# Performance work log

Measured on AMD Instinct MI355X. Metric: run time of the kernel, lower is better.

The kernel has to match this reference:

```python
import jax, jax.numpy as jnp
import numpy as np

S, B, D, H, DH = 512, 32, 256, 8, 32  # seq, batch, in_dim, heads, dim_head
LN_EPS = 1e-5


def setup_inputs() -> dict:
    key = jax.random.key(0)
    k1, k2, k3 = jax.random.split(key, 3)
    x = jax.random.normal(k1, (S, B, D), jnp.float32)
    slow_W = jax.random.normal(k2, (H * (5 * DH + 2), D), jnp.float32) * 0.02
    out_W = jax.random.normal(k3, (D, H * DH), jnp.float32) * 0.02
    ln_g = jnp.ones((D,), jnp.float32)
    ln_b = jnp.zeros((D,), jnp.float32)
    return {"x": x, "slow_W": slow_W, "out_W": out_W, "ln_g": ln_g, "ln_b": ln_b}


def elu_p1(x):
    return jax.nn.elu(x) + 1.0


def sum_norm(x):
    return x / jnp.sum(x, axis=-1, keepdims=True)


def layer_norm(x, g, b):
    mu = jnp.mean(x, axis=-1, keepdims=True)
    var = jnp.mean(jnp.square(x - mu), axis=-1, keepdims=True)
    return (x - mu) * jax.lax.rsqrt(var + LN_EPS) * g + b


def _fast_rnn_forward(x, slow_W, out_W, ln_g, ln_b):
    slen, bsz, _ = x.shape
    o = layer_norm(x, ln_g, ln_b)
    qkv = jnp.einsum('sbd,ed->sbe', o, slow_W)  # [S,B,H*(5*DH+2)]
    qkv = qkv.reshape(slen, bsz, H, 5 * DH + 2)
    q, k, v, rk, rv, beta, rbeta = jnp.split(
        qkv, [DH, 2 * DH, 3 * DH, 4 * DH, 5 * DH, 5 * DH + 1], axis=-1)
    beta = jax.nn.sigmoid(beta)      # [S,B,H,1]
    rbeta = jax.nn.sigmoid(rbeta)    # [S,B,H,1]
    q = sum_norm(elu_p1(q))
    k = sum_norm(elu_p1(k))
    rk = jax.nn.softmax(rk, axis=-1)

    # ---- feed-forward fast weights with delta rule (fast_weight_delta) ----
    def ff_step(W, inp):
        qt, kt, vt, bt = inp                      # [B,H,DH], bt [B,H,1]
        v_old = jnp.einsum('bhij,bhj->bhi', W, kt)
        W = W + ((bt * (vt - v_old))[..., :, None] * kt[..., None, :])
        z = jnp.einsum('bhij,bhj->bhi', W, qt)
        return W, z

    W0 = jnp.zeros((bsz, H, DH, DH), x.dtype)
    _, z = jax.lax.scan(ff_step, W0, (q, k, v, beta))  # z: [S,B,H,DH]

    # ---- recurrent fast weights (fast_rnn_v2): query = softmax(prev state) ----
    def rec_step(carry, inp):
        R, h = carry
        zt, kt, vt, bt = inp
        q_rec = jax.nn.softmax(h, axis=-1)         # query from previous state
        v_old = jnp.einsum('bhij,bhj->bhi', R, kt)
        R = R + ((bt * (vt - v_old))[..., :, None] * kt[..., None, :])
        h = zt + jnp.einsum('bhij,bhj->bhi', R, q_rec)
        return (R, h), h

    R0 = jnp.zeros((bsz, H, DH, DH), x.dtype)
    h0 = jnp.zeros((bsz, H, DH), x.dtype)
    _, hs = jax.lax.scan(rec_step, (R0, h0), (z, rk, rv, rbeta))  # [S,B,H,DH]

    out = hs.reshape(slen, bsz, H * DH)
    out = jnp.einsum('sbe,de->sbd', out, out_W)
    return x + out  # dropout is identity in eval


def reference(x, slow_W, out_W, ln_g, ln_b):
    return _fast_rnn_forward(x, slow_W, out_W, ln_g, ln_b)
```

## Files before the change

kernel.cpp:

```cpp
#include <hip/hip_runtime.h>
#include <hip/hip_bf16.h>
#include <math.h>

#define S_   512
#define B_   32
#define D_   256
#define H_   8
#define DH_  32
#define E_   (H_*(5*DH_+2))
#define SB_  (S_*B_)
#define LN_EPSF 1e-5f

#define ROWP_ 164
#define CH2_  32
#define NC2_  (S_/CH2_)
#define NPAD_ 1344

typedef short  bf16x8 __attribute__((ext_vector_type(8)));
typedef float  f32x4  __attribute__((ext_vector_type(4)));

__device__ __forceinline__ float wave_sum64(float v){
  #pragma unroll
  for (int m = 32; m >= 1; m >>= 1) v += __shfl_xor(v, m, 64);
  return v;
}
__device__ __forceinline__ float gsum32(float v){
  #pragma unroll
  for (int m = 16; m >= 1; m >>= 1) v += __shfl_xor(v, m, 32);
  return v;
}
__device__ __forceinline__ float gmax32(float v){
  #pragma unroll
  for (int m = 16; m >= 1; m >>= 1) v = fmaxf(v, __shfl_xor(v, m, 32));
  return v;
}

#if __has_builtin(__builtin_amdgcn_permlane32_swap)
typedef int v2i_ __attribute__((ext_vector_type(2)));
__device__ __forceinline__ float xhalf_sum(float x){
  v2i_ r = __builtin_amdgcn_permlane32_swap(__float_as_int(x), __float_as_int(x), false, false);
  return __int_as_float(r.x) + __int_as_float(r.y);
}
#else
__device__ __forceinline__ float xhalf_sum(float x){
  return x + __shfl_xor(x, 32, 64);
}
#endif

__device__ __forceinline__ void gl16(const float* g, float* l){
  __builtin_amdgcn_global_load_lds(
      (const __attribute__((address_space(1))) unsigned int*)g,
      (__attribute__((address_space(3))) unsigned int*)l, 16, 0, 0);
}
__device__ __forceinline__ void stage_plane32(const float* gb, int fieldOff,
                                              float* plane, int lane){
  const int tt = lane >> 3, dd = (lane & 7) << 2;
  #pragma unroll
  for (int i = 0; i < 4; i++)
    gl16(gb + (size_t)(8*i + tt)*ROWP_ + fieldOff + dd, plane + i*256);
}
__device__ __forceinline__ void stage_beta32(const float* gb, float* bpl, int lane){
  if (lane < CH2_) gl16(gb + (size_t)lane*ROWP_ + 5*DH_, bpl);
}

__global__ __launch_bounds__(256) void ln_kernel(const float* __restrict__ x,
                                                 const float* __restrict__ g,
                                                 const float* __restrict__ b,
                                                 __hip_bfloat16* __restrict__ o){
  __shared__ float sbuf[4];
  const int row = blockIdx.x, tid = threadIdx.x;
  const float v = x[(size_t)row*D_ + tid];
  float s = wave_sum64(v);
  if ((tid & 63) == 0) sbuf[tid >> 6] = s;
  __syncthreads();
  const float mu = (sbuf[0]+sbuf[1]+sbuf[2]+sbuf[3]) * (1.f/D_);
  __syncthreads();
  const float d = v - mu;
  float s2 = wave_sum64(d*d);
  if ((tid & 63) == 0) sbuf[tid >> 6] = s2;
  __syncthreads();
  const float var = (sbuf[0]+sbuf[1]+sbuf[2]+sbuf[3]) * (1.f/D_);
  const float rstd = rsqrtf(var + LN_EPSF);
  o[(size_t)row*D_ + tid] = __float2bfloat16(d*rstd*g[tid] + b[tid]);
}

__global__ __launch_bounds__(256) void cvt_w1(const float* __restrict__ W,
                                              __hip_bfloat16* __restrict__ o){
  const int r = blockIdx.x, c = threadIdx.x;
  const float v = (r < E_) ? W[(size_t)r*D_ + c] : 0.f;
  o[(size_t)r*D_ + c] = __float2bfloat16(v);
}
__global__ __launch_bounds__(256) void cvt_w2(const float* __restrict__ W,
                                              __hip_bfloat16* __restrict__ o){
  const size_t i = (size_t)blockIdx.x*256 + threadIdx.x;
  o[i] = __float2bfloat16(W[i]);
}

__global__ __launch_bounds__(256) void gemm1_mfma(const __hip_bfloat16* __restrict__ A,
                                                  const __hip_bfloat16* __restrict__ Bw,
                                                  float* __restrict__ qkvT){
  const int tid = threadIdx.x;
  const int w = tid >> 6, l = tid & 63;
  const int lr = l & 15, lk = (l >> 4) << 3;
  const int m0 = blockIdx.y*64 + (w>>1)*32;
  const int n0 = blockIdx.x*64 + (w&1)*32;

  const __hip_bfloat16* Ap = A  + (size_t)(m0+lr)*D_ + lk;
  const __hip_bfloat16* Bp = Bw + (size_t)(n0+lr)*D_ + lk;

  f32x4 acc00={0,0,0,0}, acc01={0,0,0,0}, acc10={0,0,0,0}, acc11={0,0,0,0};
  #pragma unroll
  for (int ks = 0; ks < 8; ++ks){
    const bf16x8 a0 = *(const bf16x8*)(Ap + ks*32);
    const bf16x8 a1 = *(const bf16x8*)(Ap + 16*D_ + ks*32);
    const bf16x8 b0 = *(const bf16x8*)(Bp + ks*32);
    const bf16x8 b1 = *(const bf16x8*)(Bp + 16*D_ + ks*32);
    acc00 = __builtin_amdgcn_mfma_f32_16x16x32_bf16(a0, b0, acc00, 0,0,0);
    acc01 = __builtin_amdgcn_mfma_f32_16x16x32_bf16(a0, b1, acc01, 0,0,0);
    acc10 = __builtin_amdgcn_mfma_f32_16x16x32_bf16(a1, b0, acc10, 0,0,0);
    acc11 = __builtin_amdgcn_mfma_f32_16x16x32_bf16(a1, b1, acc11, 0,0,0);
  }

  const int mrow = (l>>4)<<2;
  #pragma unroll
  for (int i=0;i<2;i++){
    #pragma unroll
    for (int j=0;j<2;j++){
      const f32x4 av = (i==0) ? (j==0?acc00:acc01) : (j==0?acc10:acc11);
      const int n = n0 + j*16 + lr;
      if (n < E_){
        const unsigned head = (unsigned)n / 162u;
        const unsigned jj   = (unsigned)n - head*162u;
        #pragma unroll
        for (int reg=0;reg<4;reg++){
          const int m = m0 + i*16 + mrow + reg;
          const int s = m >> 5, bq = m & 31;
          qkvT[((size_t)(bq*8u+head)*S_ + s)*ROWP_ + jj] = av[reg];
        }
      }
    }
  }
}

__global__ __launch_bounds__(256) void gemm2_mfma(const __hip_bfloat16* __restrict__ A,
                                                  const __hip_bfloat16* __restrict__ Bw,
                                                  const float* __restrict__ X,
                                                  float* __restrict__ C){
  const int tid = threadIdx.x;
  const int w = tid >> 6, l = tid & 63;
  const int lr = l & 15, lk = (l >> 4) << 3;
  const int m0 = blockIdx.y*64 + (w>>1)*32;
  const int n0 = blockIdx.x*64 + (w&1)*32;

  const __hip_bfloat16* Ap = A  + (size_t)(m0+lr)*D_ + lk;
  const __hip_bfloat16* Bp = Bw + (size_t)(n0+lr)*D_ + lk;

  f32x4 acc00={0,0,0,0}, acc01={0,0,0,0}, acc10={0,0,0,0}, acc11={0,0,0,0};
  #pragma unroll
  for (int ks = 0; ks < 8; ++ks){
    const bf16x8 a0 = *(const bf16x8*)(Ap + ks*32);
    const bf16x8 a1 = *(const bf16x8*)(Ap + 16*D_ + ks*32);
    const bf16x8 b0 = *(const bf16x8*)(Bp + ks*32);
    const bf16x8 b1 = *(const bf16x8*)(Bp + 16*D_ + ks*32);
    acc00 = __builtin_amdgcn_mfma_f32_16x16x32_bf16(a0, b0, acc00, 0,0,0);
    acc01 = __builtin_amdgcn_mfma_f32_16x16x32_bf16(a0, b1, acc01, 0,0,0);
    acc10 = __builtin_amdgcn_mfma_f32_16x16x32_bf16(a1, b0, acc10, 0,0,0);
    acc11 = __builtin_amdgcn_mfma_f32_16x16x32_bf16(a1, b1, acc11, 0,0,0);
  }

  const int mrow = (l>>4)<<2;
  #pragma unroll
  for (int i=0;i<2;i++){
    #pragma unroll
    for (int j=0;j<2;j++){
      const f32x4 av = (i==0) ? (j==0?acc00:acc01) : (j==0?acc10:acc11);
      const int n = n0 + j*16 + lr;
      #pragma unroll
      for (int reg=0;reg<4;reg++){
        const size_t m = (size_t)(m0 + i*16 + mrow + reg);
        C[m*D_ + n] = av[reg] + X[m*D_ + n];
      }
    }
  }
}

__global__ __launch_bounds__(256) void act2_kernel(float* __restrict__ qkvT){
  const int row = blockIdx.x*8 + (threadIdx.x >> 5);
  const int i = threadIdx.x & 31;
  float* base = qkvT + (size_t)row*ROWP_;
  float qv  = base[i];
  float kv  = base[DH_ + i];
  float rkv = base[3*DH_ + i];
  qv = qv > 0.f ? qv + 1.f : __expf(qv);
  kv = kv > 0.f ? kv + 1.f : __expf(kv);
  const float qs = gsum32(qv);
  const float ks = gsum32(kv);
  const float rm = gmax32(rkv);
  const float re = __expf(rkv - rm);
  const float rs = gsum32(re);
  base[i]         = qv / qs;
  base[DH_ + i]   = kv / ks;
  base[3*DH_ + i] = re / rs;
  if (i < 2){
    const float bv = base[5*DH_ + i];
    base[5*DH_ + i] = 1.f/(1.f + __expf(-bv));
  }
}

__global__ __launch_bounds__(64,1) void ff_scan(float* __restrict__ qkvT){
  const int pair = blockIdx.x;
  const int lane = threadIdx.x;
  const int r = lane & 31, p = lane >> 5;
  float* gbase = qkvT + (size_t)pair*S_*ROWP_;

  __shared__ __align__(16) float Lq[2][CH2_][DH_];
  __shared__ __align__(16) float Lk[2][CH2_][DH_];
  __shared__ __align__(16) float Lv[2][CH2_][DH_];
  __shared__ __align__(16) float Lb[2][CH2_][4];

  float W[16];
  #pragma unroll
  for (int i=0;i<16;i++) W[i]=0.f;

  stage_plane32(gbase, 0,      &Lq[0][0][0], lane);
  stage_plane32(gbase, DH_,    &Lk[0][0][0], lane);
  stage_plane32(gbase, 2*DH_,  &Lv[0][0][0], lane);
  stage_beta32 (gbase,         &Lb[0][0][0], lane);
  asm volatile("s_waitcnt vmcnt(0)" ::: "memory");

  for (int c = 0; c < NC2_; ++c){
    const int bi = c & 1;
    if (c+1 < NC2_){
      const float* gnext = gbase + (size_t)(c+1)*CH2_*ROWP_;
      stage_plane32(gnext, 0,     &Lq[bi^1][0][0], lane);
      stage_plane32(gnext, DH_,   &Lk[bi^1][0][0], lane);
      stage_plane32(gnext, 2*DH_, &Lv[bi^1][0][0], lane);
      stage_beta32 (gnext,        &Lb[bi^1][0][0], lane);
    }
    float* zrow0 = gbase + (size_t)c*CH2_*ROWP_;
    #pragma unroll 4
    for (int t = 0; t < CH2_; ++t){
      float q[16], k[16];
      #pragma unroll
      for (int j=0;j<4;j++){
        *(float4*)&q[4*j] = *(const float4*)&Lq[bi][t][p*16 + 4*j];
        *(float4*)&k[4*j] = *(const float4*)&Lk[bi][t][p*16 + 4*j];
      }
      const float vv = Lv[bi][t][r];
      const float bb = Lb[bi][t][0];

      float a0=0.f,a1=0.f,a2=0.f,a3=0.f;
      #pragma unroll
      for (int c4=0;c4<16;c4+=4){
        a0=fmaf(W[c4+0],k[c4+0],a0); a1=fmaf(W[c4+1],k[c4+1],a1);
        a2=fmaf(W[c4+2],k[c4+2],a2); a3=fmaf(W[c4+3],k[c4+3],a3);
      }
      const float dot1 = xhalf_sum((a0+a1)+(a2+a3));
      const float coef = bb*(vv - dot1);

      float b0=0.f,b1=0.f,b2=0.f,b3=0.f;
      #pragma unroll
      for (int c4=0;c4<16;c4+=4){
        W[c4+0]=fmaf(coef,k[c4+0],W[c4+0]); b0=fmaf(W[c4+0],q[c4+0],b0);
        W[c4+1]=fmaf(coef,k[c4+1],W[c4+1]); b1=fmaf(W[c4+1],q[c4+1],b1);
        W[c4+2]=fmaf(coef,k[c4+2],W[c4+2]); b2=fmaf(W[c4+2],q[c4+2],b2);
        W[c4+3]=fmaf(coef,k[c4+3],W[c4+3]); b3=fmaf(W[c4+3],q[c4+3],b3);
      }
      const float z = xhalf_sum((b0+b1)+(b2+b3));
      if (!p) zrow0[(size_t)t*ROWP_ + r] = z;
    }
    asm volatile("s_waitcnt vmcnt(0)" ::: "memory");
  }
}

__global__ __launch_bounds__(64,1) void rec_scan(const float* __restrict__ qkvT,
                                                 __hip_bfloat16* __restrict__ hsb){
  const int pair = blockIdx.x;
  const int lane = threadIdx.x;
  const int r = lane & 31, p = lane >> 5;
  const int b = pair >> 3, hh = pair & 7;
  const float* gbase = qkvT + (size_t)pair*S_*ROWP_;

  __shared__ __align__(16) float Lrk[2][CH2_][DH_];
  __shared__ __align__(16) float Lrv[2][CH2_][DH_];
  __shared__ __align__(16) float Lz [2][CH2_][DH_];
  __shared__ __align__(16) float Lb [2][CH2_][4];
  __shared__ __align__(16) float ebuf[2][DH_];

  float R[16];
  #pragma unroll
  for (int i=0;i<16;i++) R[i]=0.f;
  float h = 0.f;

  stage_plane32(gbase, 3*DH_, &Lrk[0][0][0], lane);
  stage_plane32(gbase, 4*DH_, &Lrv[0][0][0], lane);
  stage_plane32(gbase, 0,     &Lz [0][0][0], lane);
  stage_beta32 (gbase,        &Lb [0][0][0], lane);
  asm volatile("s_waitcnt vmcnt(0)" ::: "memory");

  for (int c = 0; c < NC2_; ++c){
    const int bi = c & 1;
    if (c+1 < NC2_){
      const float* gnext = gbase + (size_t)(c+1)*CH2_*ROWP_;
      stage_plane32(gnext, 3*DH_, &Lrk[bi^1][0][0], lane);
      stage_plane32(gnext, 4*DH_, &Lrv[bi^1][0][0], lane);
      stage_plane32(gnext, 0,     &Lz [bi^1][0][0], lane);
      stage_beta32 (gnext,        &Lb [bi^1][0][0], lane);
    }
    const int s0 = c*CH2_;
    #pragma unroll 4
    for (int t = 0; t < CH2_; ++t){
      const float e = __expf(h);
      if (!p) ebuf[t&1][r] = e;

      float k[16];
      #pragma unroll
      for (int j=0;j<4;j++)
        *(float4*)&k[4*j] = *(const float4*)&Lrk[bi][t][p*16 + 4*j];
      const float vv = Lrv[bi][t][r];
      const float zz = Lz [bi][t][r];
      const float bb = Lb [bi][t][1];

      float a0=0.f,a1=0.f,a2=0.f,a3=0.f;
      #pragma unroll
      for (int c4=0;c4<16;c4+=4){
        a0=fmaf(R[c4+0],k[c4+0],a0); a1=fmaf(R[c4+1],k[c4+1],a1);
        a2=fmaf(R[c4+2],k[c4+2],a2); a3=fmaf(R[c4+3],k[c4+3],a3);
      }
      const float dot1 = xhalf_sum((a0+a1)+(a2+a3));
      const float coef = bb*(vv - dot1);
      #pragma unroll
      for (int c4=0;c4<16;c4+=4){
        R[c4+0]=fmaf(coef,k[c4+0],R[c4+0]); R[c4+1]=fmaf(coef,k[c4+1],R[c4+1]);
        R[c4+2]=fmaf(coef,k[c4+2],R[c4+2]); R[c4+3]=fmaf(coef,k[c4+3],R[c4+3]);
      }

      float ev[16];
      #pragma unroll
      for (int j=0;j<4;j++)
        *(float4*)&ev[4*j] = *(const float4*)&ebuf[t&1][p*16 + 4*j];

      float t0=(ev[0]+ev[1])+(ev[2]+ev[3]),   t1=(ev[4]+ev[5])+(ev[6]+ev[7]);
      float t2=(ev[8]+ev[9])+(ev[10]+ev[11]), t3=(ev[12]+ev[13])+(ev[14]+ev[15]);
      const float Ss = xhalf_sum((t0+t1)+(t2+t3));

      float d0=0.f,d1=0.f,d2=0.f,d3=0.f;
      #pragma unroll
      for (int c4=0;c4<16;c4+=4){
        d0=fmaf(R[c4+0],ev[c4+0],d0); d1=fmaf(R[c4+1],ev[c4+1],d1);
        d2=fmaf(R[c4+2],ev[c4+2],d2); d3=fmaf(R[c4+3],ev[c4+3],d3);
      }
      const float dot2 = xhalf_sum((d0+d1)+(d2+d3));

      h = fmaf(dot2, __builtin_amdgcn_rcpf(Ss), zz);
      if (!p) hsb[((size_t)(s0+t)*B_ + b)*D_ + hh*DH_ + r] = __float2bfloat16(h);
    }
    asm volatile("s_waitcnt vmcnt(0)" ::: "memory");
  }
}

extern "C" void kernel_launch(void* const* d_in, const int* in_sizes, int n_in,
                              void* d_out, int out_size, void* d_ws, size_t ws_size,
                              hipStream_t stream) {
  const float* x      = (const float*)d_in[0];
  const float* slow_W = (const float*)d_in[1];
  const float* out_W  = (const float*)d_in[2];
  const float* ln_g   = (const float*)d_in[3];
  const float* ln_b   = (const float*)d_in[4];
  float* out = (float*)d_out;

  float* qkvT = (float*)d_ws;
  __hip_bfloat16* obf  = (__hip_bfloat16*)(qkvT + (size_t)B_*H_*S_*ROWP_);
  __hip_bfloat16* hsb  = obf;
  __hip_bfloat16* w1bf = obf + (size_t)SB_*D_;
  __hip_bfloat16* w2bf = w1bf + (size_t)NPAD_*D_;

  cvt_w1<<<NPAD_, 256, 0, stream>>>(slow_W, w1bf);
  cvt_w2<<<D_, 256, 0, stream>>>(out_W, w2bf);
  ln_kernel<<<SB_, 256, 0, stream>>>(x, ln_g, ln_b, obf);

  dim3 g1(NPAD_/64, SB_/64);
  gemm1_mfma<<<g1, 256, 0, stream>>>(obf, w1bf, qkvT);

  act2_kernel<<<B_*H_*S_/8, 256, 0, stream>>>(qkvT);

  ff_scan<<<B_*H_, 64, 0, stream>>>(qkvT);
  rec_scan<<<B_*H_, 64, 0, stream>>>(qkvT, hsb);

  dim3 g2(D_/64, SB_/64);
  gemm2_mfma<<<g2, 256, 0, stream>>>(hsb, w2bf, x, out);
}
```

Before: 444.9 us.

## Fuse feed-forward and recurrent fast-weight scans into one kernel

```diff
diff --git a/kernel.cpp b/kernel.cpp
--- a/kernel.cpp
+++ b/kernel.cpp
@@ -207,132 +207,93 @@
   }
 }
 
-__global__ __launch_bounds__(64,1) void ff_scan(float* __restrict__ qkvT){
-  const int pair = blockIdx.x;
-  const int lane = threadIdx.x;
-  const int r = lane & 31, p = lane >> 5;
-  float* gbase = qkvT + (size_t)pair*S_*ROWP_;
-
-  __shared__ __align__(16) float Lq[2][CH2_][DH_];
-  __shared__ __align__(16) float Lk[2][CH2_][DH_];
-  __shared__ __align__(16) float Lv[2][CH2_][DH_];
-  __shared__ __align__(16) float Lb[2][CH2_][4];
-
-  float W[16];
-  #pragma unroll
-  for (int i=0;i<16;i++) W[i]=0.f;
-
-  stage_plane32(gbase, 0,      &Lq[0][0][0], lane);
-  stage_plane32(gbase, DH_,    &Lk[0][0][0], lane);
-  stage_plane32(gbase, 2*DH_,  &Lv[0][0][0], lane);
-  stage_beta32 (gbase,         &Lb[0][0][0], lane);
-  asm volatile("s_waitcnt vmcnt(0)" ::: "memory");
-
-  for (int c = 0; c < NC2_; ++c){
-    const int bi = c & 1;
-    if (c+1 < NC2_){
-      const float* gnext = gbase + (size_t)(c+1)*CH2_*ROWP_;
-      stage_plane32(gnext, 0,     &Lq[bi^1][0][0], lane);
-      stage_plane32(gnext, DH_,   &Lk[bi^1][0][0], lane);
-      stage_plane32(gnext, 2*DH_, &Lv[bi^1][0][0], lane);
-      stage_beta32 (gnext,        &Lb[bi^1][0][0], lane);
-    }
-    float* zrow0 = gbase + (size_t)c*CH2_*ROWP_;
-    #pragma unroll 4
-    for (int t = 0; t < CH2_; ++t){
-      float q[16], k[16];
-      #pragma unroll
-      for (int j=0;j<4;j++){
-        *(float4*)&q[4*j] = *(const float4*)&Lq[bi][t][p*16 + 4*j];
-        *(float4*)&k[4*j] = *(const float4*)&Lk[bi][t][p*16 + 4*j];
-      }
-      const float vv = Lv[bi][t][r];
-      const float bb = Lb[bi][t][0];
-
-      float a0=0.f,a1=0.f,a2=0.f,a3=0.f;
-      #pragma unroll
-      for (int c4=0;c4<16;c4+=4){
-        a0=fmaf(W[c4+0],k[c4+0],a0); a1=fmaf(W[c4+1],k[c4+1],a1);
-        a2=fmaf(W[c4+2],k[c4+2],a2); a3=fmaf(W[c4+3],k[c4+3],a3);
-      }
-      const float dot1 = xhalf_sum((a0+a1)+(a2+a3));
-      const float coef = bb*(vv - dot1);
-
-      float b0=0.f,b1=0.f,b2=0.f,b3=0.f;
-      #pragma unroll
-      for (int c4=0;c4<16;c4+=4){
-        W[c4+0]=fmaf(coef,k[c4+0],W[c4+0]); b0=fmaf(W[c4+0],q[c4+0],b0);
-        W[c4+1]=fmaf(coef,k[c4+1],W[c4+1]); b1=fmaf(W[c4+1],q[c4+1],b1);
-        W[c4+2]=fmaf(coef,k[c4+2],W[c4+2]); b2=fmaf(W[c4+2],q[c4+2],b2);
-        W[c4+3]=fmaf(coef,k[c4+3],W[c4+3]); b3=fmaf(W[c4+3],q[c4+3],b3);
-      }
-      const float z = xhalf_sum((b0+b1)+(b2+b3));
-      if (!p) zrow0[(size_t)t*ROWP_ + r] = z;
-    }
-    asm volatile("s_waitcnt vmcnt(0)" ::: "memory");
-  }
-}
-
-__global__ __launch_bounds__(64,1) void rec_scan(const float* __restrict__ qkvT,
-                                                 __hip_bfloat16* __restrict__ hsb){
+__global__ __launch_bounds__(64,1) void scan_fused(const float* __restrict__ qkvT,
+                                                   __hip_bfloat16* __restrict__ hsb){
   const int pair = blockIdx.x;
   const int lane = threadIdx.x;
   const int r = lane & 31, p = lane >> 5;
   const int b = pair >> 3, hh = pair & 7;
   const float* gbase = qkvT + (size_t)pair*S_*ROWP_;
 
+  __shared__ __align__(16) float Lq [2][CH2_][DH_];
+  __shared__ __align__(16) float Lk [2][CH2_][DH_];
+  __shared__ __align__(16) float Lv [2][CH2_][DH_];
   __shared__ __align__(16) float Lrk[2][CH2_][DH_];
   __shared__ __align__(16) float Lrv[2][CH2_][DH_];
-  __shared__ __align__(16) float Lz [2][CH2_][DH_];
   __shared__ __align__(16) float Lb [2][CH2_][4];
   __shared__ __align__(16) float ebuf[2][DH_];
 
-  float R[16];
-  #pragma unroll
-  for (int i=0;i<16;i++) R[i]=0.f;
+  float W[16], R[16];
+  #pragma unroll
+  for (int i=0;i<16;i++){ W[i]=0.f; R[i]=0.f; }
   float h = 0.f;
 
-  stage_plane32(gbase, 3*DH_, &Lrk[0][0][0], lane);
-  stage_plane32(gbase, 4*DH_, &Lrv[0][0][0], lane);
-  stage_plane32(gbase, 0,     &Lz [0][0][0], lane);
-  stage_beta32 (gbase,        &Lb [0][0][0], lane);
+  stage_plane32(gbase, 0,      &Lq [0][0][0], lane);
+  stage_plane32(gbase, DH_,    &Lk [0][0][0], lane);
+  stage_plane32(gbase, 2*DH_,  &Lv [0][0][0], lane);
+  stage_plane32(gbase, 3*DH_,  &Lrk[0][0][0], lane);
+  stage_plane32(gbase, 4*DH_,  &Lrv[0][0][0], lane);
+  stage_beta32 (gbase,         &Lb [0][0][0], lane);
   asm volatile("s_waitcnt vmcnt(0)" ::: "memory");
 
   for (int c = 0; c < NC2_; ++c){
     const int bi = c & 1;
     if (c+1 < NC2_){
       const float* gnext = gbase + (size_t)(c+1)*CH2_*ROWP_;
-      stage_plane32(gnext, 3*DH_, &Lrk[bi^1][0][0], lane);
-      stage_plane32(gnext, 4*DH_, &Lrv[bi^1][0][0], lane);
-      stage_plane32(gnext, 0,     &Lz [bi^1][0][0], lane);
-      stage_beta32 (gnext,        &Lb [bi^1][0][0], lane);
+      stage_plane32(gnext, 0,      &Lq [bi^1][0][0], lane);
+      stage_plane32(gnext, DH_,    &Lk [bi^1][0][0], lane);
+      stage_plane32(gnext, 2*DH_,  &Lv [bi^1][0][0], lane);
+      stage_plane32(gnext, 3*DH_,  &Lrk[bi^1][0][0], lane);
+      stage_plane32(gnext, 4*DH_,  &Lrv[bi^1][0][0], lane);
+      stage_beta32 (gnext,         &Lb [bi^1][0][0], lane);
     }
     const int s0 = c*CH2_;
-    #pragma unroll 4
+    #pragma unroll 2
     for (int t = 0; t < CH2_; ++t){
       const float e = __expf(h);
       if (!p) ebuf[t&1][r] = e;
 
-      float k[16];
-      #pragma unroll
-      for (int j=0;j<4;j++)
-        *(float4*)&k[4*j] = *(const float4*)&Lrk[bi][t][p*16 + 4*j];
-      const float vv = Lrv[bi][t][r];
-      const float zz = Lz [bi][t][r];
-      const float bb = Lb [bi][t][1];
+      float q[16], k[16], rk[16];
+      #pragma unroll
+      for (int j=0;j<4;j++){
+        *(float4*)&q[4*j]  = *(const float4*)&Lq [bi][t][p*16 + 4*j];
+        *(float4*)&k[4*j]  = *(const float4*)&Lk [bi][t][p*16 + 4*j];
+        *(float4*)&rk[4*j] = *(const float4*)&Lrk[bi][t][p*16 + 4*j];
+      }
+      const float vv  = Lv [bi][t][r];
+      const float rvv = Lrv[bi][t][r];
+      const float2 bet = *(const float2*)&Lb[bi][t][0];
 
       float a0=0.f,a1=0.f,a2=0.f,a3=0.f;
       #pragma unroll
       for (int c4=0;c4<16;c4+=4){
-        a0=fmaf(R[c4+0],k[c4+0],a0); a1=fmaf(R[c4+1],k[c4+1],a1);
-        a2=fmaf(R[c4+2],k[c4+2],a2); a3=fmaf(R[c4+3],k[c4+3],a3);
-      }
-      const float dot1 = xhalf_sum((a0+a1)+(a2+a3));
-      const float coef = bb*(vv - dot1);
-      #pragma unroll
-      for (int c4=0;c4<16;c4+=4){
-        R[c4+0]=fmaf(coef,k[c4+0],R[c4+0]); R[c4+1]=fmaf(coef,k[c4+1],R[c4+1]);
-        R[c4+2]=fmaf(coef,k[c4+2],R[c4+2]); R[c4+3]=fmaf(coef,k[c4+3],R[c4+3]);
+        a0=fmaf(W[c4+0],k[c4+0],a0); a1=fmaf(W[c4+1],k[c4+1],a1);
+        a2=fmaf(W[c4+2],k[c4+2],a2); a3=fmaf(W[c4+3],k[c4+3],a3);
+      }
+      const float dot1f = xhalf_sum((a0+a1)+(a2+a3));
+      const float coeff = bet.x*(vv - dot1f);
+      float b0=0.f,b1=0.f,b2=0.f,b3=0.f;
+      #pragma unroll
+      for (int c4=0;c4<16;c4+=4){
+        W[c4+0]=fmaf(coeff,k[c4+0],W[c4+0]); b0=fmaf(W[c4+0],q[c4+0],b0);
+        W[c4+1]=fmaf(coeff,k[c4+1],W[c4+1]); b1=fmaf(W[c4+1],q[c4+1],b1);
+        W[c4+2]=fmaf(coeff,k[c4+2],W[c4+2]); b2=fmaf(W[c4+2],q[c4+2],b2);
+        W[c4+3]=fmaf(coeff,k[c4+3],W[c4+3]); b3=fmaf(W[c4+3],q[c4+3],b3);
+      }
+      const float z = xhalf_sum((b0+b1)+(b2+b3));
+
+      float c0=0.f,c1=0.f,c2=0.f,c3=0.f;
+      #pragma unroll
+      for (int c4=0;c4<16;c4+=4){
+        c0=fmaf(R[c4+0],rk[c4+0],c0); c1=fmaf(R[c4+1],rk[c4+1],c1);
+        c2=fmaf(R[c4+2],rk[c4+2],c2); c3=fmaf(R[c4+3],rk[c4+3],c3);
+      }
+      const float dot1r = xhalf_sum((c0+c1)+(c2+c3));
+      const float coefr = bet.y*(rvv - dot1r);
+      #pragma unroll
+      for (int c4=0;c4<16;c4+=4){
+        R[c4+0]=fmaf(coefr,rk[c4+0],R[c4+0]); R[c4+1]=fmaf(coefr,rk[c4+1],R[c4+1]);
+        R[c4+2]=fmaf(coefr,rk[c4+2],R[c4+2]); R[c4+3]=fmaf(coefr,rk[c4+3],R[c4+3]);
       }
 
       float ev[16];
@@ -352,7 +313,7 @@
       }
       const float dot2 = xhalf_sum((d0+d1)+(d2+d3));
 
-      h = fmaf(dot2, __builtin_amdgcn_rcpf(Ss), zz);
+      h = fmaf(dot2, __builtin_amdgcn_rcpf(Ss), z);
       if (!p) hsb[((size_t)(s0+t)*B_ + b)*D_ + hh*DH_ + r] = __float2bfloat16(h);
     }
     asm volatile("s_waitcnt vmcnt(0)" ::: "memory");
@@ -384,8 +345,7 @@
 
   act2_kernel<<<B_*H_*S_/8, 256, 0, stream>>>(qkvT);
 
-  ff_scan<<<B_*H_, 64, 0, stream>>>(qkvT);
-  rec_scan<<<B_*H_, 64, 0, stream>>>(qkvT, hsb);
+  scan_fused<<<B_*H_, 64, 0, stream>>>(qkvT, hsb);
 
   dim3 g2(D_/64, SB_/64);
   gemm2_mfma<<<g2, 256, 0, stream>>>(hsb, w2bf, x, out);
```

New measurement: 419.2 us. -5.8%, faster.
